# Kernel tuning notes

Hardware: AMD Instinct MI355X
Metric: run time of the kernel (lower is better)

The kernel has to match this reference:

```python
import jax, jax.numpy as jnp
import numpy as np

N, K, T, F = 256, 64, 128, 64  # n_samples, n_clusters, seq_len, n_features
ALPHA = 1.0


def setup_inputs() -> dict:
    key = jax.random.key(0)
    k1, k2 = jax.random.split(key)
    return {
        "inputs": jax.random.normal(k1, (N, T, F), dtype=jnp.float32),
        "clusters": jax.random.normal(k2, (K, T, F), dtype=jnp.float32),
    }


def _soft_kmeans(inputs, clusters, alpha=ALPHA):
    # Euclidean branch: distance = sqrt( sum_t (x - c)^2 ).sum over features
    # Expand the time reduction as x2 + c2 - 2*x.c to avoid the (N,K,T,F) tensor.
    x2 = jnp.sum(inputs * inputs, axis=1)                      # (N, F)
    c2 = jnp.sum(clusters * clusters, axis=1)                  # (K, F)
    xc = jnp.einsum('ntf,ktf->nkf', inputs, clusters)          # (N, K, F)
    d2 = jnp.maximum(x2[:, None, :] + c2[None, :, :] - 2.0 * xc, 0.0)
    distance = jnp.sqrt(d2).sum(-1)                            # (N, K)

    q = 1.0 / (1.0 + (distance * distance) / alpha)
    q = q ** ((alpha + 1.0) / 2.0)
    q = jax.nn.softmax(q, axis=1)                              # (N, K)
    p = jax.nn.softmax((q * q) / q.sum(0), axis=1)             # (N, K)
    # Faithful to nn.KLDivLoss(reduction='batchmean')(p, q):
    #   input p is treated as log-probs -> sum(q * (log q - p)) / N
    loss = jnp.sum(q * (jnp.log(q) - p)) / q.shape[0]
    return q, loss


def reference(inputs, clusters):
    return _soft_kmeans(inputs, clusters)
```

## Files before the change

### kernel.cpp

```cpp
#include <hip/hip_runtime.h>
#include <stdint.h>

#define N_S 256
#define K_C 64
#define T_L 128
#define F_D 64

typedef short short8 __attribute__((ext_vector_type(8)));
typedef float float4v __attribute__((ext_vector_type(4)));

__global__ __launch_bounds__(256) void k_convert(
    const float* __restrict__ x, const float* __restrict__ c,
    uint16_t* __restrict__ xb, uint16_t* __restrict__ cb,
    float* __restrict__ x2, float* __restrict__ c2)
{
    const int tid  = threadIdx.x;
    const int lane = tid & 63;
    const int w    = tid >> 6;
    const int b    = blockIdx.x;

    const float* src;
    uint16_t*    dst;
    float*       sq;
    if (b < 64) {
        const int row = b * 4 + w;
        src = x + (size_t)row * T_L * F_D;
        dst = xb + (size_t)lane * N_S * T_L + (size_t)row * T_L;
        sq  = x2 + row * F_D + lane;
    } else {
        const int row = (b - 64) * 4 + w;
        src = c + (size_t)row * T_L * F_D;
        dst = cb + (size_t)lane * K_C * T_L + (size_t)row * T_L;
        sq  = c2 + row * F_D + lane;
    }

    float acc = 0.f;
    for (int t0 = 0; t0 < T_L; t0 += 8) {
        union { uint16_t h[8]; uint4 v; } buf;
        #pragma unroll
        for (int j = 0; j < 8; ++j) {
            float v = src[(t0 + j) * F_D + lane];
            acc = fmaf(v, v, acc);
            uint32_t u = __float_as_uint(v);
            uint32_t r = (u + 0x7FFFu + ((u >> 16) & 1u)) >> 16;
            buf.h[j] = (uint16_t)r;
        }
        *reinterpret_cast<uint4*>(dst + t0) = buf.v;
    }
    *sq = acc;
}

__global__ __launch_bounds__(512) void k_dist(
    const uint16_t* __restrict__ xb, const uint16_t* __restrict__ cb,
    const float* __restrict__ x2, const float* __restrict__ c2,
    float* __restrict__ dist)
{
    const int tid  = threadIdx.x;
    const int lane = tid & 63;
    const int w    = tid >> 6;
    const int nt   = blockIdx.x >> 2;
    const int kt   = blockIdx.x & 3;
    const int n0   = nt * 16, k0 = kt * 16;
    const int row  = lane & 15;
    const int tg   = lane >> 4;
    const int f0   = w * 8;

    __shared__ float red[8][16][17];

    float dsum[4] = {0.f, 0.f, 0.f, 0.f};

    const uint16_t* abase = xb + (size_t)(n0 + row) * T_L + (size_t)tg * 8;
    const uint16_t* bbase = cb + (size_t)(k0 + row) * T_L + (size_t)tg * 8;

    #pragma unroll
    for (int f = 0; f < 8; ++f) {
        const int ff = f0 + f;
        const short8* ap = reinterpret_cast<const short8*>(abase + (size_t)ff * N_S * T_L);
        const short8* bp = reinterpret_cast<const short8*>(bbase + (size_t)ff * K_C * T_L);
        float4v acc = {0.f, 0.f, 0.f, 0.f};
        #pragma unroll
        for (int ts = 0; ts < 4; ++ts) {
            short8 a = ap[ts * 4];
            short8 bfr = bp[ts * 4];
            acc = __builtin_amdgcn_mfma_f32_16x16x32_bf16(a, bfr, acc, 0, 0, 0);
        }
        const float c2v = c2[(k0 + row) * F_D + ff];
        #pragma unroll
        for (int r = 0; r < 4; ++r) {
            const int m = tg * 4 + r;
            const float x2v = x2[(n0 + m) * F_D + ff];
            float d2 = fmaf(-2.0f, acc[r], x2v + c2v);
            dsum[r] += sqrtf(fmaxf(d2, 0.f));
        }
    }

    #pragma unroll
    for (int r = 0; r < 4; ++r) red[w][tg * 4 + r][row] = dsum[r];
    __syncthreads();

    if (tid < 256) {
        const int m = tid >> 4, kl = tid & 15;
        float s = 0.f;
        #pragma unroll
        for (int ww = 0; ww < 8; ++ww) s += red[ww][m][kl];
        dist[(n0 + m) * K_C + (k0 + kl)] = s;
    }
}

__global__ __launch_bounds__(256) void k_softmax(
    const float* __restrict__ dist, float* __restrict__ q,
    float* __restrict__ colsum)
{
    const int tid  = threadIdx.x;
    const int lane = tid & 63;
    const int w    = tid >> 6;
    const int n    = blockIdx.x * 4 + w;

    const float d = dist[n * K_C + lane];
    const float v = 1.0f / fmaf(d, d, 1.0f);

    float m = v;
    #pragma unroll
    for (int off = 32; off; off >>= 1) m = fmaxf(m, __shfl_xor(m, off));
    const float e = __expf(v - m);
    float s = e;
    #pragma unroll
    for (int off = 32; off; off >>= 1) s += __shfl_xor(s, off);
    const float qv = e / s;

    q[n * K_C + lane] = qv;

    __shared__ float part[4][64];
    part[w][lane] = qv;
    __syncthreads();
    if (tid < 64) {
        float t = part[0][tid] + part[1][tid] + part[2][tid] + part[3][tid];
        atomicAdd(&colsum[tid], t);
    }
}

__global__ __launch_bounds__(256) void k_loss(
    const float* __restrict__ q, const float* __restrict__ colsum,
    float* __restrict__ loss)
{
    const int tid  = threadIdx.x;
    const int lane = tid & 63;
    const int w    = tid >> 6;
    const int n    = blockIdx.x * 4 + w;

    const float qv = q[n * K_C + lane];
    const float s  = qv * qv / colsum[lane];

    float m = s;
    #pragma unroll
    for (int off = 32; off; off >>= 1) m = fmaxf(m, __shfl_xor(m, off));
    const float e = __expf(s - m);
    float se = e;
    #pragma unroll
    for (int off = 32; off; off >>= 1) se += __shfl_xor(se, off);
    const float p = e / se;

    float term = qv * (__logf(qv) - p);
    #pragma unroll
    for (int off = 32; off; off >>= 1) term += __shfl_xor(term, off);

    __shared__ float part[4];
    if (lane == 0) part[w] = term;
    __syncthreads();
    if (tid == 0) {
        const float t = (part[0] + part[1] + part[2] + part[3]) * (1.0f / N_S);
        atomicAdd(loss, t);
    }
}

extern "C" void kernel_launch(void* const* d_in, const int* in_sizes, int n_in,
                              void* d_out, int out_size, void* d_ws, size_t ws_size,
                              hipStream_t stream)
{
    const float* x = (const float*)d_in[0];
    const float* c = (const float*)d_in[1];
    float* out = (float*)d_out;

    char* ws = (char*)d_ws;
    uint16_t* xb     = (uint16_t*)(ws);
    uint16_t* cb     = (uint16_t*)(ws + 4194304);
    float*    x2     = (float*)(ws + 5242880);
    float*    c2     = (float*)(ws + 5308416);
    float*    dist   = (float*)(ws + 5324800);
    float*    colsum = (float*)(ws + 5390336);

    float* q    = out;
    float* loss = out + 16384;

    hipMemsetAsync(colsum, 0, K_C * sizeof(float), stream);
    hipMemsetAsync(loss, 0, sizeof(float), stream);

    k_convert<<<80, 256, 0, stream>>>(x, c, xb, cb, x2, c2);
    k_dist   <<<64, 512, 0, stream>>>(xb, cb, x2, c2, dist);
    k_softmax<<<64, 256, 0, stream>>>(dist, q, colsum);
    k_loss   <<<64, 256, 0, stream>>>(q, colsum, loss);
}
```

Measured before the change: 95.92 us.

## Fuse softmax and loss kernels into one single-block tail kernel

Replaces the separate softmax and loss kernels with a single 1024-thread block that computes q, the column sums in shared memory, and the KL loss in one pass. This removes two memset launches, one kernel launch, and the global atomics for colsum and loss. In exchange the whole tail runs on one CU with 16 rows per wave processed serially, so it gives up parallelism across the GPU.

New measurement: 108.4 us. +13.0%, slower.

```diff
diff --git a/kernel.cpp b/kernel.cpp
--- a/kernel.cpp
+++ b/kernel.cpp
@@ -107,69 +107,75 @@
     }
 }
 
-__global__ __launch_bounds__(256) void k_softmax(
+__global__ __launch_bounds__(1024) void k_tail(
     const float* __restrict__ dist, float* __restrict__ q,
-    float* __restrict__ colsum)
+    float* __restrict__ loss)
 {
     const int tid  = threadIdx.x;
     const int lane = tid & 63;
     const int w    = tid >> 6;
-    const int n    = blockIdx.x * 4 + w;
-
-    const float d = dist[n * K_C + lane];
-    const float v = 1.0f / fmaf(d, d, 1.0f);
-
-    float m = v;
+
+    __shared__ float q_s[N_S][K_C];
+    __shared__ float part[16][K_C];
+    __shared__ float colsum_s[K_C];
+    __shared__ float lpart[16];
+
+    for (int r = 0; r < 16; ++r) {
+        const int row = w * 16 + r;
+        const float d = dist[row * K_C + lane];
+        const float v = 1.0f / fmaf(d, d, 1.0f);
+        float m = v;
+        #pragma unroll
+        for (int off = 32; off; off >>= 1) m = fmaxf(m, __shfl_xor(m, off));
+        const float e = __expf(v - m);
+        float s = e;
+        #pragma unroll
+        for (int off = 32; off; off >>= 1) s += __shfl_xor(s, off);
+        const float qv = e / s;
+        q[row * K_C + lane] = qv;
+        q_s[row][lane] = qv;
+    }
+    __syncthreads();
+
+    {
+        float acc = 0.f;
+        #pragma unroll
+        for (int r = 0; r < 16; ++r) acc += q_s[w * 16 + r][lane];
+        part[w][lane] = acc;
+    }
+    __syncthreads();
+    if (tid < K_C) {
+        float acc = 0.f;
+        #pragma unroll
+        for (int g = 0; g < 16; ++g) acc += part[g][tid];
+        colsum_s[tid] = acc;
+    }
+    __syncthreads();
+
+    float tsum = 0.f;
+    for (int r = 0; r < 16; ++r) {
+        const int row = w * 16 + r;
+        const float qv = q_s[row][lane];
+        const float s  = qv * qv / colsum_s[lane];
+        float m = s;
+        #pragma unroll
+        for (int off = 32; off; off >>= 1) m = fmaxf(m, __shfl_xor(m, off));
+        const float e = __expf(s - m);
+        float se = e;
+        #pragma unroll
+        for (int off = 32; off; off >>= 1) se += __shfl_xor(se, off);
+        const float p = e / se;
+        tsum += qv * (__logf(qv) - p);
+    }
     #pragma unroll
-    for (int off = 32; off; off >>= 1) m = fmaxf(m, __shfl_xor(m, off));
-    const float e = __expf(v - m);
-    float s = e;
-    #pragma unroll
-    for (int off = 32; off; off >>= 1) s += __shfl_xor(s, off);
-    const float qv = e / s;
-
-    q[n * K_C + lane] = qv;
-
-    __shared__ float part[4][64];
-    part[w][lane] = qv;
-    __syncthreads();
-    if (tid < 64) {
-        float t = part[0][tid] + part[1][tid] + part[2][tid] + part[3][tid];
-        atomicAdd(&colsum[tid], t);
-    }
-}
-
-__global__ __launch_bounds__(256) void k_loss(
-    const float* __restrict__ q, const float* __restrict__ colsum,
-    float* __restrict__ loss)
-{
-    const int tid  = threadIdx.x;
-    const int lane = tid & 63;
-    const int w    = tid >> 6;
-    const int n    = blockIdx.x * 4 + w;
-
-    const float qv = q[n * K_C + lane];
-    const float s  = qv * qv / colsum[lane];
-
-    float m = s;
-    #pragma unroll
-    for (int off = 32; off; off >>= 1) m = fmaxf(m, __shfl_xor(m, off));
-    const float e = __expf(s - m);
-    float se = e;
-    #pragma unroll
-    for (int off = 32; off; off >>= 1) se += __shfl_xor(se, off);
-    const float p = e / se;
-
-    float term = qv * (__logf(qv) - p);
-    #pragma unroll
-    for (int off = 32; off; off >>= 1) term += __shfl_xor(term, off);
-
-    __shared__ float part[4];
-    if (lane == 0) part[w] = term;
+    for (int off = 32; off; off >>= 1) tsum += __shfl_xor(tsum, off);
+    if (lane == 0) lpart[w] = tsum;
     __syncthreads();
     if (tid == 0) {
-        const float t = (part[0] + part[1] + part[2] + part[3]) * (1.0f / N_S);
-        atomicAdd(loss, t);
+        float t = 0.f;
+        #pragma unroll
+        for (int g = 0; g < 16; ++g) t += lpart[g];
+        loss[0] = t * (1.0f / N_S);
     }
 }
 
@@ -187,16 +193,11 @@
     float*    x2     = (float*)(ws + 5242880);
     float*    c2     = (float*)(ws + 5308416);
     float*    dist   = (float*)(ws + 5324800);
-    float*    colsum = (float*)(ws + 5390336);
 
     float* q    = out;
     float* loss = out + 16384;
 
-    hipMemsetAsync(colsum, 0, K_C * sizeof(float), stream);
-    hipMemsetAsync(loss, 0, sizeof(float), stream);
-
     k_convert<<<80, 256, 0, stream>>>(x, c, xb, cb, x2, c2);
     k_dist   <<<64, 512, 0, stream>>>(xb, cb, x2, c2, dist);
-    k_softmax<<<64, 256, 0, stream>>>(dist, q, colsum);
-    k_loss   <<<64, 256, 0, stream>>>(q, colsum, loss);
-}
+    k_tail   <<<1, 1024, 0, stream>>>(dist, q, loss);
+}
```

## Fuse all four stages into one cooperative kernel with grid syncs

Applied to the files above, without the earlier changes.

Replaces the two memsets and four separate launches with a single cooperative kernel of 64 blocks. Grid-wide barriers separate the convert, distance, softmax and loss phases. The workspace zeroing moves into block 0, and the q values are kept in shared memory for the loss phase. This removes per-launch overhead and the memset calls, but it adds three grid.sync barriers and reduces the convert phase to 64 blocks with 8 waves each.

Result: slower. 136.6 us (+42.4%).

```diff
diff --git a/kernel.cpp b/kernel.cpp
--- a/kernel.cpp
+++ b/kernel.cpp
@@ -1,5 +1,8 @@
 #include <hip/hip_runtime.h>
+#include <hip/hip_cooperative_groups.h>
 #include <stdint.h>
+
+namespace cg = cooperative_groups;
 
 #define N_S 256
 #define K_C 64
@@ -9,166 +12,144 @@
 typedef short short8 __attribute__((ext_vector_type(8)));
 typedef float float4v __attribute__((ext_vector_type(4)));
 
-__global__ __launch_bounds__(256) void k_convert(
+__global__ __launch_bounds__(512) void k_fused(
     const float* __restrict__ x, const float* __restrict__ c,
     uint16_t* __restrict__ xb, uint16_t* __restrict__ cb,
-    float* __restrict__ x2, float* __restrict__ c2)
+    float* __restrict__ x2, float* __restrict__ c2,
+    float* __restrict__ dist, float* __restrict__ colsum,
+    float* __restrict__ q, float* __restrict__ loss)
 {
+    cg::grid_group grid = cg::this_grid();
     const int tid  = threadIdx.x;
     const int lane = tid & 63;
     const int w    = tid >> 6;
-    const int b    = blockIdx.x;
-
-    const float* src;
-    uint16_t*    dst;
-    float*       sq;
-    if (b < 64) {
-        const int row = b * 4 + w;
-        src = x + (size_t)row * T_L * F_D;
-        dst = xb + (size_t)lane * N_S * T_L + (size_t)row * T_L;
-        sq  = x2 + row * F_D + lane;
-    } else {
-        const int row = (b - 64) * 4 + w;
-        src = c + (size_t)row * T_L * F_D;
-        dst = cb + (size_t)lane * K_C * T_L + (size_t)row * T_L;
-        sq  = c2 + row * F_D + lane;
-    }
-
-    float acc = 0.f;
-    for (int t0 = 0; t0 < T_L; t0 += 8) {
-        union { uint16_t h[8]; uint4 v; } buf;
-        #pragma unroll
-        for (int j = 0; j < 8; ++j) {
-            float v = src[(t0 + j) * F_D + lane];
-            acc = fmaf(v, v, acc);
-            uint32_t u = __float_as_uint(v);
-            uint32_t r = (u + 0x7FFFu + ((u >> 16) & 1u)) >> 16;
-            buf.h[j] = (uint16_t)r;
-        }
-        *reinterpret_cast<uint4*>(dst + t0) = buf.v;
-    }
-    *sq = acc;
-}
-
-__global__ __launch_bounds__(512) void k_dist(
-    const uint16_t* __restrict__ xb, const uint16_t* __restrict__ cb,
-    const float* __restrict__ x2, const float* __restrict__ c2,
-    float* __restrict__ dist)
-{
-    const int tid  = threadIdx.x;
-    const int lane = tid & 63;
-    const int w    = tid >> 6;
-    const int nt   = blockIdx.x >> 2;
-    const int kt   = blockIdx.x & 3;
-    const int n0   = nt * 16, k0 = kt * 16;
-    const int row  = lane & 15;
-    const int tg   = lane >> 4;
-    const int f0   = w * 8;
+    const int blk  = blockIdx.x;
 
     __shared__ float red[8][16][17];
+    __shared__ float q_s[4][K_C];
+    __shared__ float part[4][K_C];
+    __shared__ float lpart[4];
 
-    float dsum[4] = {0.f, 0.f, 0.f, 0.f};
-
-    const uint16_t* abase = xb + (size_t)(n0 + row) * T_L + (size_t)tg * 8;
-    const uint16_t* bbase = cb + (size_t)(k0 + row) * T_L + (size_t)tg * 8;
-
-    #pragma unroll
-    for (int f = 0; f < 8; ++f) {
-        const int ff = f0 + f;
-        const short8* ap = reinterpret_cast<const short8*>(abase + (size_t)ff * N_S * T_L);
-        const short8* bp = reinterpret_cast<const short8*>(bbase + (size_t)ff * K_C * T_L);
-        float4v acc = {0.f, 0.f, 0.f, 0.f};
-        #pragma unroll
-        for (int ts = 0; ts < 4; ++ts) {
-            short8 a = ap[ts * 4];
-            short8 bfr = bp[ts * 4];
-            acc = __builtin_amdgcn_mfma_f32_16x16x32_bf16(a, bfr, acc, 0, 0, 0);
+    {
+        const int g = blk * 8 + w;
+        if (g < 320) {
+            const float* src; uint16_t* dst; float* sq;
+            if (g < 256) {
+                src = x + (size_t)g * T_L * F_D;
+                dst = xb + (size_t)lane * N_S * T_L + (size_t)g * T_L;
+                sq  = x2 + g * F_D + lane;
+            } else {
+                const int row = g - 256;
+                src = c + (size_t)row * T_L * F_D;
+                dst = cb + (size_t)lane * K_C * T_L + (size_t)row * T_L;
+                sq  = c2 + row * F_D + lane;
+            }
+            float acc = 0.f;
+            for (int t0 = 0; t0 < T_L; t0 += 8) {
+                union { uint16_t h[8]; uint4 v; } buf;
+                #pragma unroll
+                for (int j = 0; j < 8; ++j) {
+                    float v = src[(t0 + j) * F_D + lane];
+                    acc = fmaf(v, v, acc);
+                    uint32_t u = __float_as_uint(v);
+                    uint32_t r = (u + 0x7FFFu + ((u >> 16) & 1u)) >> 16;
+                    buf.h[j] = (uint16_t)r;
+                }
+                *reinterpret_cast<uint4*>(dst + t0) = buf.v;
+            }
+            *sq = acc;
         }
-        const float c2v = c2[(k0 + row) * F_D + ff];
-        #pragma unroll
-        for (int r = 0; r < 4; ++r) {
-            const int m = tg * 4 + r;
-            const float x2v = x2[(n0 + m) * F_D + ff];
-            float d2 = fmaf(-2.0f, acc[r], x2v + c2v);
-            dsum[r] += sqrtf(fmaxf(d2, 0.f));
+        if (blk == 0) {
+            if (tid < K_C) colsum[tid] = 0.f;
+            if (tid == K_C) loss[0] = 0.f;
         }
     }
+    grid.sync();
 
-    #pragma unroll
-    for (int r = 0; r < 4; ++r) red[w][tg * 4 + r][row] = dsum[r];
+    {
+        const int nt  = blk >> 2, kt = blk & 3;
+        const int n0  = nt * 16, k0 = kt * 16;
+        const int row = lane & 15;
+        const int tg  = lane >> 4;
+        const int f0  = w * 8;
+
+        float dsum[4] = {0.f, 0.f, 0.f, 0.f};
+        const uint16_t* abase = xb + (size_t)(n0 + row) * T_L + (size_t)tg * 8;
+        const uint16_t* bbase = cb + (size_t)(k0 + row) * T_L + (size_t)tg * 8;
+
+        #pragma unroll
+        for (int f = 0; f < 8; ++f) {
+            const int ff = f0 + f;
+            const short8* ap = reinterpret_cast<const short8*>(abase + (size_t)ff * N_S * T_L);
+            const short8* bp = reinterpret_cast<const short8*>(bbase + (size_t)ff * K_C * T_L);
+            float4v acc = {0.f, 0.f, 0.f, 0.f};
+            #pragma unroll
+            for (int ts = 0; ts < 4; ++ts)
+                acc = __builtin_amdgcn_mfma_f32_16x16x32_bf16(ap[ts * 4], bp[ts * 4], acc, 0, 0, 0);
+            const float c2v = c2[(k0 + row) * F_D + ff];
+            #pragma unroll
+            for (int r = 0; r < 4; ++r) {
+                const int m = tg * 4 + r;
+                const float x2v = x2[(n0 + m) * F_D + ff];
+                float d2 = fmaf(-2.0f, acc[r], x2v + c2v);
+                dsum[r] += sqrtf(fmaxf(d2, 0.f));
+            }
+        }
+        #pragma unroll
+        for (int r = 0; r < 4; ++r) red[w][tg * 4 + r][row] = dsum[r];
+        __syncthreads();
+        if (tid < 256) {
+            const int m = tid >> 4, kl = tid & 15;
+            float s = 0.f;
+            #pragma unroll
+            for (int ww = 0; ww < 8; ++ww) s += red[ww][m][kl];
+            dist[(n0 + m) * K_C + (k0 + kl)] = s;
+        }
+    }
+    grid.sync();
+
+    if (w < 4) {
+        const int row = blk * 4 + w;
+        const float d = dist[row * K_C + lane];
+        const float v = 1.0f / fmaf(d, d, 1.0f);
+        float m = v;
+        #pragma unroll
+        for (int off = 32; off; off >>= 1) m = fmaxf(m, __shfl_xor(m, off));
+        const float e = __expf(v - m);
+        float s = e;
+        #pragma unroll
+        for (int off = 32; off; off >>= 1) s += __shfl_xor(s, off);
+        const float qv = e / s;
+        q[row * K_C + lane] = qv;
+        q_s[w][lane]  = qv;
+        part[w][lane] = qv;
+    }
     __syncthreads();
+    if (tid < K_C) {
+        const float s = part[0][tid] + part[1][tid] + part[2][tid] + part[3][tid];
+        atomicAdd(&colsum[tid], s);
+    }
+    grid.sync();
 
-    if (tid < 256) {
-        const int m = tid >> 4, kl = tid & 15;
-        float s = 0.f;
+    if (w < 4) {
+        const float qv = q_s[w][lane];
+        const float s  = qv * qv / colsum[lane];
+        float m = s;
         #pragma unroll
-        for (int ww = 0; ww < 8; ++ww) s += red[ww][m][kl];
-        dist[(n0 + m) * K_C + (k0 + kl)] = s;
+        for (int off = 32; off; off >>= 1) m = fmaxf(m, __shfl_xor(m, off));
+        const float e = __expf(s - m);
+        float se = e;
+        #pragma unroll
+        for (int off = 32; off; off >>= 1) se += __shfl_xor(se, off);
+        const float p = e / se;
+        float term = qv * (__logf(qv) - p);
+        #pragma unroll
+        for (int off = 32; off; off >>= 1) term += __shfl_xor(term, off);
+        if (lane == 0) lpart[w] = term;
     }
-}
-
-__global__ __launch_bounds__(256) void k_softmax(
-    const float* __restrict__ dist, float* __restrict__ q,
-    float* __restrict__ colsum)
-{
-    const int tid  = threadIdx.x;
-    const int lane = tid & 63;
-    const int w    = tid >> 6;
-    const int n    = blockIdx.x * 4 + w;
-
-    const float d = dist[n * K_C + lane];
-    const float v = 1.0f / fmaf(d, d, 1.0f);
-
-    float m = v;
-    #pragma unroll
-    for (int off = 32; off; off >>= 1) m = fmaxf(m, __shfl_xor(m, off));
-    const float e = __expf(v - m);
-    float s = e;
-    #pragma unroll
-    for (int off = 32; off; off >>= 1) s += __shfl_xor(s, off);
-    const float qv = e / s;
-
-    q[n * K_C + lane] = qv;
-
-    __shared__ float part[4][64];
-    part[w][lane] = qv;
-    __syncthreads();
-    if (tid < 64) {
-        float t = part[0][tid] + part[1][tid] + part[2][tid] + part[3][tid];
-        atomicAdd(&colsum[tid], t);
-    }
-}
-
-__global__ __launch_bounds__(256) void k_loss(
-    const float* __restrict__ q, const float* __restrict__ colsum,
-    float* __restrict__ loss)
-{
-    const int tid  = threadIdx.x;
-    const int lane = tid & 63;
-    const int w    = tid >> 6;
-    const int n    = blockIdx.x * 4 + w;
-
-    const float qv = q[n * K_C + lane];
-    const float s  = qv * qv / colsum[lane];
-
-    float m = s;
-    #pragma unroll
-    for (int off = 32; off; off >>= 1) m = fmaxf(m, __shfl_xor(m, off));
-    const float e = __expf(s - m);
-    float se = e;
-    #pragma unroll
-    for (int off = 32; off; off >>= 1) se += __shfl_xor(se, off);
-    const float p = e / se;
-
-    float term = qv * (__logf(qv) - p);
-    #pragma unroll
-    for (int off = 32; off; off >>= 1) term += __shfl_xor(term, off);
-
-    __shared__ float part[4];
-    if (lane == 0) part[w] = term;
     __syncthreads();
     if (tid == 0) {
-        const float t = (part[0] + part[1] + part[2] + part[3]) * (1.0f / N_S);
+        const float t = (lpart[0] + lpart[1] + lpart[2] + lpart[3]) * (1.0f / N_S);
         atomicAdd(loss, t);
     }
 }
@@ -192,11 +173,10 @@
     float* q    = out;
     float* loss = out + 16384;
 
-    hipMemsetAsync(colsum, 0, K_C * sizeof(float), stream);
-    hipMemsetAsync(loss, 0, sizeof(float), stream);
-
-    k_convert<<<80, 256, 0, stream>>>(x, c, xb, cb, x2, c2);
-    k_dist   <<<64, 512, 0, stream>>>(xb, cb, x2, c2, dist);
-    k_softmax<<<64, 256, 0, stream>>>(dist, q, colsum);
-    k_loss   <<<64, 256, 0, stream>>>(q, colsum, loss);
+    void* args[] = {
+        (void*)&x, (void*)&c, (void*)&xb, (void*)&cb, (void*)&x2, (void*)&c2,
+        (void*)&dist, (void*)&colsum, (void*)&q, (void*)&loss
+    };
+    hipLaunchCooperativeKernel((const void*)k_fused, dim3(64), dim3(512),
+                               args, 0, stream);
 }
```
